# Performance work log

Hardware: AMD Instinct MI355X
Metric: run time of the kernel (lower is better)

Reference implementation:

```python
import jax, jax.numpy as jnp
import numpy as np

FILTER = 3
STRIDE = 1


def setup_inputs() -> dict:
    key = jax.random.key(0)
    ks = jax.random.split(key, 6)
    B, P, N, d_in, d_ein, d_model = 16, 4, 4096, 128, 32, 128
    e_dim = FILTER * (FILTER - 1) * d_ein  # 192
    adj = jax.random.uniform(ks[0], (N, N), jnp.float32)
    features = jax.random.normal(ks[1], (B, N, d_in), jnp.float32)
    edge_features = jax.random.normal(ks[2], (B, N, e_dim), jnp.float32)
    mask = jax.random.uniform(ks[3], (P, N, 1), jnp.float32)
    W = jax.random.normal(ks[4], (FILTER * d_in + e_dim, d_model), jnp.float32) * 0.02
    b = jnp.zeros((d_model,), jnp.float32)
    return dict(adj=adj, features=features, edge_features=edge_features, mask=mask, W=W, b=b)


def reference(adj, features, edge_features, mask, W, b):
    Fs, S = FILTER, STRIDE
    B, N, d_in = features.shape
    # padding rule from _padding(): below_pad = filter - (N % stride or stride)
    below_pad = N % S
    below_pad = S if below_pad == 0 else below_pad
    below_pad = Fs - below_pad  # = 2 for stride=1, filter=3
    n_out = (N + below_pad - Fs) // S + 1  # = N

    feat_pad = jnp.pad(features, ((0, 0), (0, below_pad), (0, 0)))
    idx = jnp.arange(n_out)[:, None] * S + jnp.arange(Fs)[None, :]  # [n_out, F]
    win = feat_pad[:, idx, :]  # [B, n_out, F, d_in] (gather = torch unfold windows)
    jump = win.mean(axis=2)    # features.unfold(...).sum(-1)/filter -> [B, n_out, d_in]
    # torch unfold puts filter dim last: [B, n_out, d_in, F]; flatten(-2,-1) is d_in-major
    feat_flat = jnp.swapaxes(win, -1, -2).reshape(B, n_out, Fs * d_in)

    mask_pad = jnp.pad(mask, ((0, 0), (0, below_pad), (0, 0)))
    m = mask_pad[:, idx, :].max(axis=2)  # [P, n_out, 1]

    feat_cat = jnp.concatenate([feat_flat, edge_features], axis=-1)  # [B, n_out, 576]
    out = jax.nn.relu(feat_cat @ W + b)  # dropout is identity in eval
    res = out + jump  # residual (res=True)

    P = m.shape[0]
    d_model = out.shape[-1]
    out_m = (m * out.reshape(-1, P, n_out, d_model)).reshape(-1, n_out, d_model)
    res_m = (m * res.reshape(-1, P, n_out, d_model)).reshape(-1, n_out, d_model)
    return adj, res_m, out_m, m
```

## Files before the change

### kernel.cpp

```cpp
#include <hip/hip_runtime.h>
#include <hip/hip_bf16.h>

typedef __attribute__((ext_vector_type(8))) short short8;
typedef __attribute__((ext_vector_type(4))) float floatx4;

#define NN     4096
#define DIN    128
#define EDIM   192
#define DMODEL 128

__device__ __forceinline__ unsigned short f2bf(float f) {
    union { float f; unsigned int i; } x; x.f = f;
    unsigned int u = x.i;
    u += 0x7FFFu + ((u >> 16) & 1u);
    return (unsigned short)(u >> 16);
}

__device__ __forceinline__ unsigned int pk2(float lo, float hi) {
    union { __hip_bfloat162 v; unsigned int u; } cv;
    cv.v = __float22bfloat162_rn(make_float2(lo, hi));
    return cv.u;
}

__device__ __forceinline__ short8 cvt8(const float4 a, const float4 b) {
    union { short8 s; unsigned int u[4]; } r;
    r.u[0] = pk2(a.x, a.y);
    r.u[1] = pk2(a.z, a.w);
    r.u[2] = pk2(b.x, b.y);
    r.u[3] = pk2(b.z, b.w);
    return r.s;
}

__device__ __forceinline__ void gl_lds16(const void* g, void* l) {
    __builtin_amdgcn_global_load_lds(
        (const __attribute__((address_space(1))) unsigned int*)g,
        (__attribute__((address_space(3))) unsigned int*)l,
        16, 0, 0);
}

__global__ void prep_w(const float* __restrict__ W, unsigned short* __restrict__ wf) {
    const int t = blockIdx.x * 256 + threadIdx.x;
    const int jj   = t & 7;
    const int lane = (t >> 3) & 63;
    const int ct   = (t >> 9) & 7;
    const int gs   = t >> 12;
    const int kt = gs * 32 + ((lane >> 4) << 3) + jj;
    const int korig = (kt < 384) ? ((kt & 127) * 3 + (kt >> 7)) : kt;
    const int n = ct * 16 + (lane & 15);
    wf[t] = f2bf(W[korig * DMODEL + n]);
}

__global__ __launch_bounds__(256, 2) void main_k(
    const float* __restrict__ feat,
    const float* __restrict__ edgef,
    const unsigned short* __restrict__ wfrag,
    const float* __restrict__ bias,
    const float* __restrict__ mask,
    const floatx4* __restrict__ adj4,
    floatx4* __restrict__ o_adj4,
    float* __restrict__ o_res,
    float* __restrict__ o_out,
    float* __restrict__ o_m)
{
    __shared__ __align__(16) char lbuf[2][8192];
    __shared__ float m3s[128];

    const int tid  = threadIdx.x;
    const int lane = tid & 63;
    const int wv   = tid >> 6;
    const int nn   = lane & 15;
    const int quad = lane >> 4;

    const int blk = blockIdx.x;
    const int b   = blk >> 5;
    const int i0  = (blk & 31) << 7;
    const int p   = b & 3;

    const float* fb = feat  + (size_t)b * NN * DIN;
    const float* eb = edgef + (size_t)b * NN * EDIM;
    const int rowb = i0 + wv * 32 + nn;

    if (tid < 128) {
        const int i = i0 + tid;
        float v = mask[p * NN + i];
        if (i + 1 < NN) v = fmaxf(v, mask[p * NN + i + 1]);
        if (i + 2 < NN) v = fmaxf(v, mask[p * NN + i + 2]);
        m3s[tid] = v;
        if (b < 4) o_m[p * NN + i] = v;
    }

    const char* wsrc = (const char*)wfrag;

    auto stageB = [&](int s, int bi) {
        const char* src = wsrc + s * 8192 + wv * 2048 + lane * 16;
        char* dst = &lbuf[bi][wv * 2048];
        gl_lds16(src, dst);
        gl_lds16(src + 1024, dst + 1024);
    };

    const float4 zf4 = make_float4(0.f, 0.f, 0.f, 0.f);

    auto loadA = [&](int s, float4& a00, float4& a01, float4& a10, float4& a11) {
        if (s < 12) {
            const int j = s >> 2, sl = s & 3;
            const int off = sl * 32 + quad * 8;
            const int r0 = rowb + j;
            a00 = zf4; a01 = zf4;
            if (r0 < NN) {
                const float* sp = fb + (size_t)r0 * DIN + off;
                a00 = *(const float4*)sp; a01 = *(const float4*)(sp + 4);
            }
            const int r1 = rowb + 16 + j;
            a10 = zf4; a11 = zf4;
            if (r1 < NN) {
                const float* sp = fb + (size_t)r1 * DIN + off;
                a10 = *(const float4*)sp; a11 = *(const float4*)(sp + 4);
            }
        } else {
            const int eg = s - 12;
            const int off = eg * 32 + quad * 8;
            const float* sp0 = eb + (size_t)rowb * EDIM + off;
            a00 = *(const float4*)sp0; a01 = *(const float4*)(sp0 + 4);
            const float* sp1 = eb + (size_t)(rowb + 16) * EDIM + off;
            a10 = *(const float4*)sp1; a11 = *(const float4*)(sp1 + 4);
        }
    };

    floatx4 acc[2][8];
    #pragma unroll
    for (int rt = 0; rt < 2; ++rt)
        #pragma unroll
        for (int ct = 0; ct < 8; ++ct)
            acc[rt][ct] = (floatx4){0.f, 0.f, 0.f, 0.f};

    float4 a00, a01, a10, a11, n00, n01, n10, n11;
    stageB(0, 0);
    loadA(0, a00, a01, a10, a11);
    __syncthreads();

    #pragma unroll
    for (int s = 0; s < 18; ++s) {
        const int cur = s & 1;
        if (s < 17) {
            stageB(s + 1, cur ^ 1);
            loadA(s + 1, n00, n01, n10, n11);
        }
        const short8* bl = (const short8*)(&lbuf[cur][0]);
        const short8 af0 = cvt8(a00, a01);
        const short8 af1 = cvt8(a10, a11);
        #pragma unroll
        for (int ct = 0; ct < 8; ++ct) {
            const short8 bfr = bl[ct * 64 + lane];
            acc[0][ct] = __builtin_amdgcn_mfma_f32_16x16x32_bf16(af0, bfr, acc[0][ct], 0, 0, 0);
            acc[1][ct] = __builtin_amdgcn_mfma_f32_16x16x32_bf16(af1, bfr, acc[1][ct], 0, 0, 0);
        }
        a00 = n00; a01 = n01; a10 = n10; a11 = n11;
        __syncthreads();
    }

    float biasv[8];
    #pragma unroll
    for (int ct = 0; ct < 8; ++ct)
        biasv[ct] = bias[ct * 16 + nn];

    const float inv3 = 1.0f / 3.0f;

    #pragma unroll
    for (int rt = 0; rt < 2; ++rt) {
        const int rbase = wv * 32 + rt * 16 + quad * 4;
        float mv[4];
        #pragma unroll
        for (int reg = 0; reg < 4; ++reg)
            mv[reg] = m3s[rbase + reg];
        #pragma unroll
        for (int ct = 0; ct < 8; ++ct) {
            const int col = ct * 16 + nn;
            float fv[6];
            #pragma unroll
            for (int t6 = 0; t6 < 6; ++t6) {
                const int row = i0 + rbase + t6;
                fv[t6] = (row < NN) ? fb[(size_t)row * DIN + col] : 0.f;
            }
            #pragma unroll
            for (int reg = 0; reg < 4; ++reg) {
                float o = acc[rt][ct][reg] + biasv[ct];
                o = fmaxf(o, 0.f);
                const float jmp = (fv[reg] + fv[reg + 1] + fv[reg + 2]) * inv3;
                const size_t off = ((size_t)b * NN + (i0 + rbase + reg)) * DMODEL + col;
                const float mm = mv[reg];
                __builtin_nontemporal_store(mm * o, &o_out[off]);
                __builtin_nontemporal_store(mm * (o + jmp), &o_res[off]);
            }
        }
    }

    {
        const int idx = blk * 256 + tid;
        #pragma unroll
        for (int i = 0; i < 32; ++i) {
            const floatx4 v = __builtin_nontemporal_load(&adj4[idx + i * 131072]);
            __builtin_nontemporal_store(v, &o_adj4[idx + i * 131072]);
        }
    }
}

extern "C" void kernel_launch(void* const* d_in, const int* in_sizes, int n_in,
                              void* d_out, int out_size, void* d_ws, size_t ws_size,
                              hipStream_t stream) {
    const float* adj   = (const float*)d_in[0];
    const float* feat  = (const float*)d_in[1];
    const float* edgef = (const float*)d_in[2];
    const float* mask  = (const float*)d_in[3];
    const float* W     = (const float*)d_in[4];
    const float* bias  = (const float*)d_in[5];

    float* out   = (float*)d_out;
    float* o_adj = out;
    float* o_res = out + (size_t)16777216;
    float* o_out = o_res + (size_t)8388608;
    float* o_m   = o_out + (size_t)8388608;

    unsigned short* wfrag = (unsigned short*)d_ws;

    prep_w<<<288, 256, 0, stream>>>(W, wfrag);
    main_k<<<512, 256, 0, stream>>>(feat, edgef, wfrag, bias, mask,
                                    (const floatx4*)adj, (floatx4*)o_adj,
                                    o_res, o_out, o_m);
}
```

Measured before the change: 272.6 us.

## Interleave adj copy into GEMM loop and load B fragments directly to registers

Removes the LDS double-buffer for weight fragments and loads B fragments straight from global (L2-resident) into registers with a two-stage register prefetch, dropping per-iteration barriers. The 64MB adj passthrough copy is spread across the 18 K-steps, so its loads and stores overlap MFMA work instead of running as a tail phase. This adds register pressure (two B stages, two A stages, four adj vectors), which may hurt occupancy or cause spills under launch_bounds(256,2).

```diff
diff --git a/kernel.cpp b/kernel.cpp
--- a/kernel.cpp
+++ b/kernel.cpp
@@ -29,13 +29,6 @@
     r.u[2] = pk2(b.x, b.y);
     r.u[3] = pk2(b.z, b.w);
     return r.s;
-}
-
-__device__ __forceinline__ void gl_lds16(const void* g, void* l) {
-    __builtin_amdgcn_global_load_lds(
-        (const __attribute__((address_space(1))) unsigned int*)g,
-        (__attribute__((address_space(3))) unsigned int*)l,
-        16, 0, 0);
 }
 
 __global__ void prep_w(const float* __restrict__ W, unsigned short* __restrict__ wf) {
@@ -62,7 +55,6 @@
     float* __restrict__ o_out,
     float* __restrict__ o_m)
 {
-    __shared__ __align__(16) char lbuf[2][8192];
     __shared__ float m3s[128];
 
     const int tid  = threadIdx.x;
@@ -79,6 +71,7 @@
     const float* fb = feat  + (size_t)b * NN * DIN;
     const float* eb = edgef + (size_t)b * NN * EDIM;
     const int rowb = i0 + wv * 32 + nn;
+    const int adjbase = blk * 256 + tid;
 
     if (tid < 128) {
         const int i = i0 + tid;
@@ -88,41 +81,44 @@
         m3s[tid] = v;
         if (b < 4) o_m[p * NN + i] = v;
     }
-
-    const char* wsrc = (const char*)wfrag;
-
-    auto stageB = [&](int s, int bi) {
-        const char* src = wsrc + s * 8192 + wv * 2048 + lane * 16;
-        char* dst = &lbuf[bi][wv * 2048];
-        gl_lds16(src, dst);
-        gl_lds16(src + 1024, dst + 1024);
+    __syncthreads();
+
+    const short8* wf8 = (const short8*)wfrag;
+    const float4 zf4 = make_float4(0.f, 0.f, 0.f, 0.f);
+
+    float4  Ar[2][4];
+    short8  Br[2][8];
+    floatx4 Ja[2], Jb[2];
+
+    auto loadB = [&](int s, short8* B) {
+        #pragma unroll
+        for (int ct = 0; ct < 8; ++ct)
+            B[ct] = wf8[(s * 8 + ct) * 64 + lane];
     };
 
-    const float4 zf4 = make_float4(0.f, 0.f, 0.f, 0.f);
-
-    auto loadA = [&](int s, float4& a00, float4& a01, float4& a10, float4& a11) {
+    auto loadA = [&](int s, float4* A) {
         if (s < 12) {
             const int j = s >> 2, sl = s & 3;
             const int off = sl * 32 + quad * 8;
             const int r0 = rowb + j;
-            a00 = zf4; a01 = zf4;
+            A[0] = zf4; A[1] = zf4;
             if (r0 < NN) {
                 const float* sp = fb + (size_t)r0 * DIN + off;
-                a00 = *(const float4*)sp; a01 = *(const float4*)(sp + 4);
+                A[0] = *(const float4*)sp; A[1] = *(const float4*)(sp + 4);
             }
             const int r1 = rowb + 16 + j;
-            a10 = zf4; a11 = zf4;
+            A[2] = zf4; A[3] = zf4;
             if (r1 < NN) {
                 const float* sp = fb + (size_t)r1 * DIN + off;
-                a10 = *(const float4*)sp; a11 = *(const float4*)(sp + 4);
+                A[2] = *(const float4*)sp; A[3] = *(const float4*)(sp + 4);
             }
         } else {
             const int eg = s - 12;
             const int off = eg * 32 + quad * 8;
             const float* sp0 = eb + (size_t)rowb * EDIM + off;
-            a00 = *(const float4*)sp0; a01 = *(const float4*)(sp0 + 4);
+            A[0] = *(const float4*)sp0; A[1] = *(const float4*)(sp0 + 4);
             const float* sp1 = eb + (size_t)(rowb + 16) * EDIM + off;
-            a10 = *(const float4*)sp1; a11 = *(const float4*)(sp1 + 4);
+            A[2] = *(const float4*)sp1; A[3] = *(const float4*)(sp1 + 4);
         }
     };
 
@@ -133,29 +129,45 @@
         for (int ct = 0; ct < 8; ++ct)
             acc[rt][ct] = (floatx4){0.f, 0.f, 0.f, 0.f};
 
-    float4 a00, a01, a10, a11, n00, n01, n10, n11;
-    stageB(0, 0);
-    loadA(0, a00, a01, a10, a11);
-    __syncthreads();
+    loadB(0, Br[0]);
+    loadB(1, Br[1]);
+    loadA(0, Ar[0]);
+    loadA(1, Ar[1]);
+    Ja[0] = __builtin_nontemporal_load(&adj4[adjbase]);
+    Jb[0] = __builtin_nontemporal_load(&adj4[adjbase + (size_t)1 * 131072]);
+    Ja[1] = __builtin_nontemporal_load(&adj4[adjbase + (size_t)2 * 131072]);
+    Jb[1] = __builtin_nontemporal_load(&adj4[adjbase + (size_t)3 * 131072]);
 
     #pragma unroll
     for (int s = 0; s < 18; ++s) {
-        const int cur = s & 1;
-        if (s < 17) {
-            stageB(s + 1, cur ^ 1);
-            loadA(s + 1, n00, n01, n10, n11);
-        }
-        const short8* bl = (const short8*)(&lbuf[cur][0]);
-        const short8 af0 = cvt8(a00, a01);
-        const short8 af1 = cvt8(a10, a11);
+        const int pr = s & 1;
+
+        const short8 af0 = cvt8(Ar[pr][0], Ar[pr][1]);
+        const short8 af1 = cvt8(Ar[pr][2], Ar[pr][3]);
+
+        if (s <= 15) {
+            __builtin_nontemporal_store(Ja[pr], &o_adj4[adjbase + (size_t)(2 * s) * 131072]);
+            __builtin_nontemporal_store(Jb[pr], &o_adj4[adjbase + (size_t)(2 * s + 1) * 131072]);
+        }
+        if (s <= 13) {
+            Ja[pr] = __builtin_nontemporal_load(&adj4[adjbase + (size_t)(2 * s + 4) * 131072]);
+            Jb[pr] = __builtin_nontemporal_load(&adj4[adjbase + (size_t)(2 * s + 5) * 131072]);
+        }
+
+        short8 bt[8];
+        #pragma unroll
+        for (int ct = 0; ct < 8; ++ct)
+            bt[ct] = Br[pr][ct];
+        if (s <= 15) {
+            loadB(s + 2, Br[pr]);
+            loadA(s + 2, Ar[pr]);
+        }
+
         #pragma unroll
         for (int ct = 0; ct < 8; ++ct) {
-            const short8 bfr = bl[ct * 64 + lane];
-            acc[0][ct] = __builtin_amdgcn_mfma_f32_16x16x32_bf16(af0, bfr, acc[0][ct], 0, 0, 0);
-            acc[1][ct] = __builtin_amdgcn_mfma_f32_16x16x32_bf16(af1, bfr, acc[1][ct], 0, 0, 0);
-        }
-        a00 = n00; a01 = n01; a10 = n10; a11 = n11;
-        __syncthreads();
+            acc[0][ct] = __builtin_amdgcn_mfma_f32_16x16x32_bf16(af0, bt[ct], acc[0][ct], 0, 0, 0);
+            acc[1][ct] = __builtin_amdgcn_mfma_f32_16x16x32_bf16(af1, bt[ct], acc[1][ct], 0, 0, 0);
+        }
     }
 
     float biasv[8];
@@ -193,15 +205,6 @@
             }
         }
     }
-
-    {
-        const int idx = blk * 256 + tid;
-        #pragma unroll
-        for (int i = 0; i < 32; ++i) {
-            const floatx4 v = __builtin_nontemporal_load(&adj4[idx + i * 131072]);
-            __builtin_nontemporal_store(v, &o_adj4[idx + i * 131072]);
-        }
-    }
 }
 
 extern "C" void kernel_launch(void* const* d_in, const int* in_sizes, int n_in,
```

Result: slower. 285.8 us (+4.8%).

## Use 512-thread blocks and interleave adj copy with GEMM k-loop

Applied to the files above, without the earlier changes.

Doubles the threads per block so each wave owns a 16-row tile instead of 32, halving per-wave accumulators and A loads to raise occupancy. The adjacency copy moves from a tail loop into the GEMM k-loop, one float4 load and store per stage, so the bulk copy traffic overlaps MFMA work and the A/B loads. In exchange each B fragment in LDS is reused by only one row tile per wave, and the interleaved copy adds memory pressure during the compute phase.

```diff
diff --git a/kernel.cpp b/kernel.cpp
--- a/kernel.cpp
+++ b/kernel.cpp
@@ -50,7 +50,7 @@
     wf[t] = f2bf(W[korig * DMODEL + n]);
 }
 
-__global__ __launch_bounds__(256, 2) void main_k(
+__global__ __launch_bounds__(512, 4) void main_k(
     const float* __restrict__ feat,
     const float* __restrict__ edgef,
     const unsigned short* __restrict__ wfrag,
@@ -78,7 +78,8 @@
 
     const float* fb = feat  + (size_t)b * NN * DIN;
     const float* eb = edgef + (size_t)b * NN * EDIM;
-    const int rowb = i0 + wv * 32 + nn;
+    const int rowb = i0 + wv * 16 + nn;
+    const int adjbase = blk * 512 + tid;
 
     if (tid < 128) {
         const int i = i0 + tid;
@@ -92,70 +93,65 @@
     const char* wsrc = (const char*)wfrag;
 
     auto stageB = [&](int s, int bi) {
-        const char* src = wsrc + s * 8192 + wv * 2048 + lane * 16;
-        char* dst = &lbuf[bi][wv * 2048];
+        const char* src = wsrc + s * 8192 + wv * 1024 + lane * 16;
+        char* dst = &lbuf[bi][wv * 1024];
         gl_lds16(src, dst);
-        gl_lds16(src + 1024, dst + 1024);
     };
 
     const float4 zf4 = make_float4(0.f, 0.f, 0.f, 0.f);
 
-    auto loadA = [&](int s, float4& a00, float4& a01, float4& a10, float4& a11) {
+    auto loadA = [&](int s, float4& a0, float4& a1) {
         if (s < 12) {
             const int j = s >> 2, sl = s & 3;
             const int off = sl * 32 + quad * 8;
-            const int r0 = rowb + j;
-            a00 = zf4; a01 = zf4;
-            if (r0 < NN) {
-                const float* sp = fb + (size_t)r0 * DIN + off;
-                a00 = *(const float4*)sp; a01 = *(const float4*)(sp + 4);
-            }
-            const int r1 = rowb + 16 + j;
-            a10 = zf4; a11 = zf4;
-            if (r1 < NN) {
-                const float* sp = fb + (size_t)r1 * DIN + off;
-                a10 = *(const float4*)sp; a11 = *(const float4*)(sp + 4);
+            const int r = rowb + j;
+            a0 = zf4; a1 = zf4;
+            if (r < NN) {
+                const float* sp = fb + (size_t)r * DIN + off;
+                a0 = *(const float4*)sp; a1 = *(const float4*)(sp + 4);
             }
         } else {
             const int eg = s - 12;
             const int off = eg * 32 + quad * 8;
-            const float* sp0 = eb + (size_t)rowb * EDIM + off;
-            a00 = *(const float4*)sp0; a01 = *(const float4*)(sp0 + 4);
-            const float* sp1 = eb + (size_t)(rowb + 16) * EDIM + off;
-            a10 = *(const float4*)sp1; a11 = *(const float4*)(sp1 + 4);
+            const float* sp = eb + (size_t)rowb * EDIM + off;
+            a0 = *(const float4*)sp; a1 = *(const float4*)(sp + 4);
         }
     };
 
-    floatx4 acc[2][8];
-    #pragma unroll
-    for (int rt = 0; rt < 2; ++rt)
+    floatx4 acc[8];
+    #pragma unroll
+    for (int ct = 0; ct < 8; ++ct)
+        acc[ct] = (floatx4){0.f, 0.f, 0.f, 0.f};
+
+    float4 a0, a1, n0, n1;
+    floatx4 Jcur, Jnxt;
+    stageB(0, 0);
+    loadA(0, a0, a1);
+    Jcur = __builtin_nontemporal_load(&adj4[adjbase]);
+    __syncthreads();
+
+    #pragma unroll
+    for (int s = 0; s < 18; ++s) {
+        const int cur = s & 1;
+
+        if (s <= 15)
+            __builtin_nontemporal_store(Jcur, &o_adj4[adjbase + (size_t)s * 262144]);
+        if (s <= 14)
+            Jnxt = __builtin_nontemporal_load(&adj4[adjbase + (size_t)(s + 1) * 262144]);
+
+        if (s < 17) {
+            stageB(s + 1, cur ^ 1);
+            loadA(s + 1, n0, n1);
+        }
+
+        const short8* bl = (const short8*)(&lbuf[cur][0]);
+        const short8 af = cvt8(a0, a1);
         #pragma unroll
         for (int ct = 0; ct < 8; ++ct)
-            acc[rt][ct] = (floatx4){0.f, 0.f, 0.f, 0.f};
-
-    float4 a00, a01, a10, a11, n00, n01, n10, n11;
-    stageB(0, 0);
-    loadA(0, a00, a01, a10, a11);
-    __syncthreads();
-
-    #pragma unroll
-    for (int s = 0; s < 18; ++s) {
-        const int cur = s & 1;
-        if (s < 17) {
-            stageB(s + 1, cur ^ 1);
-            loadA(s + 1, n00, n01, n10, n11);
-        }
-        const short8* bl = (const short8*)(&lbuf[cur][0]);
-        const short8 af0 = cvt8(a00, a01);
-        const short8 af1 = cvt8(a10, a11);
-        #pragma unroll
-        for (int ct = 0; ct < 8; ++ct) {
-            const short8 bfr = bl[ct * 64 + lane];
-            acc[0][ct] = __builtin_amdgcn_mfma_f32_16x16x32_bf16(af0, bfr, acc[0][ct], 0, 0, 0);
-            acc[1][ct] = __builtin_amdgcn_mfma_f32_16x16x32_bf16(af1, bfr, acc[1][ct], 0, 0, 0);
-        }
-        a00 = n00; a01 = n01; a10 = n10; a11 = n11;
-        __syncthreads();
+            acc[ct] = __builtin_amdgcn_mfma_f32_16x16x32_bf16(af, bl[ct * 64 + lane], acc[ct], 0, 0, 0);
+
+        a0 = n0; a1 = n1; Jcur = Jnxt;
+        if (s < 17) __syncthreads();
     }
 
     float biasv[8];
@@ -164,42 +160,30 @@
         biasv[ct] = bias[ct * 16 + nn];
 
     const float inv3 = 1.0f / 3.0f;
-
-    #pragma unroll
-    for (int rt = 0; rt < 2; ++rt) {
-        const int rbase = wv * 32 + rt * 16 + quad * 4;
-        float mv[4];
+    const int rbase = wv * 16 + quad * 4;
+    float mv[4];
+    #pragma unroll
+    for (int reg = 0; reg < 4; ++reg)
+        mv[reg] = m3s[rbase + reg];
+
+    #pragma unroll
+    for (int ct = 0; ct < 8; ++ct) {
+        const int col = ct * 16 + nn;
+        float fv[6];
         #pragma unroll
-        for (int reg = 0; reg < 4; ++reg)
-            mv[reg] = m3s[rbase + reg];
+        for (int t6 = 0; t6 < 6; ++t6) {
+            const int row = i0 + rbase + t6;
+            fv[t6] = (row < NN) ? fb[(size_t)row * DIN + col] : 0.f;
+        }
         #pragma unroll
-        for (int ct = 0; ct < 8; ++ct) {
-            const int col = ct * 16 + nn;
-            float fv[6];
-            #pragma unroll
-            for (int t6 = 0; t6 < 6; ++t6) {
-                const int row = i0 + rbase + t6;
-                fv[t6] = (row < NN) ? fb[(size_t)row * DIN + col] : 0.f;
-            }
-            #pragma unroll
-            for (int reg = 0; reg < 4; ++reg) {
-                float o = acc[rt][ct][reg] + biasv[ct];
-                o = fmaxf(o, 0.f);
-                const float jmp = (fv[reg] + fv[reg + 1] + fv[reg + 2]) * inv3;
-                const size_t off = ((size_t)b * NN + (i0 + rbase + reg)) * DMODEL + col;
-                const float mm = mv[reg];
-                __builtin_nontemporal_store(mm * o, &o_out[off]);
-                __builtin_nontemporal_store(mm * (o + jmp), &o_res[off]);
-            }
-        }
-    }
-
-    {
-        const int idx = blk * 256 + tid;
-        #pragma unroll
-        for (int i = 0; i < 32; ++i) {
-            const floatx4 v = __builtin_nontemporal_load(&adj4[idx + i * 131072]);
-            __builtin_nontemporal_store(v, &o_adj4[idx + i * 131072]);
+        for (int reg = 0; reg < 4; ++reg) {
+            float o = acc[ct][reg] + biasv[ct];
+            o = fmaxf(o, 0.f);
+            const float jmp = (fv[reg] + fv[reg + 1] + fv[reg + 2]) * inv3;
+            const size_t off = ((size_t)b * NN + (i0 + rbase + reg)) * DMODEL + col;
+            const float mm = mv[reg];
+            __builtin_nontemporal_store(mm * o, &o_out[off]);
+            __builtin_nontemporal_store(mm * (o + jmp), &o_res[off]);
         }
     }
 }
@@ -223,7 +207,7 @@
     unsigned short* wfrag = (unsigned short*)d_ws;
 
     prep_w<<<288, 256, 0, stream>>>(W, wfrag);
-    main_k<<<512, 256, 0, stream>>>(feat, edgef, wfrag, bias, mask,
+    main_k<<<512, 512, 0, stream>>>(feat, edgef, wfrag, bias, mask,
                                     (const floatx4*)adj, (floatx4*)o_adj,
                                     o_res, o_out, o_m);
 }
```

Measured after the change: 267.0 us. -2.1%, faster.
